# Performance work log

Measured on AMD Instinct MI355X. Metric: run time of the kernel, lower is better.

## Reference

```python
import jax, jax.numpy as jnp
import numpy as np

B, T, C = 2, 2048, 1024
N_HEAD = 16
HEAD_DIM = C // N_HEAD

def setup_inputs() -> dict:
    key = jax.random.key(0)
    k1, k2, k3 = jax.random.split(key, 3)
    x = jax.random.normal(k1, (B, T, C), dtype=jnp.float32)
    # Dense kernel init scale ~ 1/sqrt(fan_in) for stable softmax
    w_attn = jax.random.normal(k2, (C, 3 * C), dtype=jnp.float32) / np.sqrt(C)
    w_proj = jax.random.normal(k3, (C, C), dtype=jnp.float32) / np.sqrt(C)
    return {"x": x, "w_attn": w_attn, "w_proj": w_proj}

def reference(x, w_attn, w_proj):
    Bc, Tc, Cc = x.shape
    # QKV projection (use_bias=False)
    qkv = x @ w_attn  # [B, T, 3C]
    q, k, v = jnp.split(qkv, 3, axis=-1)
    # [B, T, C] -> [B, H, T, D]
    def heads(a):
        return a.reshape(Bc, Tc, N_HEAD, HEAD_DIM).swapaxes(1, 2)
    q, k, v = heads(q), heads(k), heads(v)
    scale = 1.0 / jnp.sqrt(jnp.asarray(HEAD_DIM, dtype=x.dtype))
    attn = jnp.einsum('bhqd,bhkd->bhqk', q, k) * scale  # [B, H, T, T]
    attn = jax.nn.softmax(attn, axis=-1)
    # dropout=0.0 / deterministic -> identity
    y = jnp.einsum('bhqk,bhkd->bhqd', attn, v)  # [B, H, T, D]
    y = y.swapaxes(1, 2).reshape(Bc, Tc, Cc)
    return y @ w_proj  # output projection, no bias, dropout identity
```

## Files before the change

kernel.cpp:

```cpp
#include <hip/hip_runtime.h>
#include <hip/hip_bf16.h>

#define B_   2
#define T_   2048
#define C_   1024
#define NH_  16
#define HD_  64

typedef __attribute__((ext_vector_type(8))) short short8;
typedef __attribute__((ext_vector_type(4))) float float4_;
typedef __attribute__((ext_vector_type(4))) _Float16 half4_;
typedef __attribute__((ext_vector_type(2))) __fp16  fp16x2;

static __device__ __forceinline__ unsigned short f2bf(float f) {
    union { float f; unsigned u; } v; v.f = f;
    unsigned r = v.u + 0x7fffu + ((v.u >> 16) & 1u);
    return (unsigned short)(r >> 16);
}
static __device__ __forceinline__ float bf2f(unsigned short b) {
    union { unsigned u; float f; } v; v.u = (unsigned)b << 16;
    return v.f;
}

static __device__ __forceinline__ void g2l16(const void* g, void* l) {
    __builtin_amdgcn_global_load_lds(
        (const __attribute__((address_space(1))) void*)g,
        (__attribute__((address_space(3))) void*)l, 16, 0, 0);
}

__global__ __launch_bounds__(256) void conv_bf16(
    const float* __restrict__ in, unsigned short* __restrict__ out, int n8)
{
    int i = blockIdx.x * 256 + threadIdx.x;
    if (i >= n8) return;
    const float4* p = (const float4*)in + (size_t)i * 2;
    float4 a = p[0], b = p[1];
    short8 o;
    o[0]=f2bf(a.x); o[1]=f2bf(a.y); o[2]=f2bf(a.z); o[3]=f2bf(a.w);
    o[4]=f2bf(b.x); o[5]=f2bf(b.y); o[6]=f2bf(b.z); o[7]=f2bf(b.w);
    *((short8*)out + i) = o;
}

__global__ __launch_bounds__(256) void tconv2(
    const float* __restrict__ inA, unsigned short* __restrict__ outA, int CcA, int ys,
    const float* __restrict__ inB, unsigned short* __restrict__ outB, int CcB)
{
    __shared__ __align__(16) unsigned short Ts[64][72];
    const int t = threadIdx.x;
    const int R = 1024;
    const float* in; unsigned short* out; int Cc, c0;
    if ((int)blockIdx.y < ys) { in = inA; out = outA; Cc = CcA; c0 = blockIdx.y * 64; }
    else                      { in = inB; out = outB; Cc = CcB; c0 = (blockIdx.y - ys) * 64; }
    const int r0 = blockIdx.x * 64;
    #pragma unroll
    for (int cc = 0; cc < 2; ++cc) {
        int c = cc * 256 + t;
        int r = c >> 3, col = (c & 7) * 8;
        const float* p = in + (size_t)(r0 + r) * Cc + c0 + col;
        #pragma unroll
        for (int i = 0; i < 8; ++i) Ts[col + i][r] = f2bf(p[i]);
    }
    __syncthreads();
    #pragma unroll
    for (int cc = 0; cc < 2; ++cc) {
        int c = cc * 256 + t;
        int cr = c >> 3, oc = (c & 7) * 8;
        uint4 v = *(const uint4*)(&Ts[cr][oc]);
        *(uint4*)(out + (size_t)(c0 + cr) * R + r0 + oc) = v;
    }
}

__global__ __launch_bounds__(256) void vtrans(
    const unsigned short* __restrict__ qkv, unsigned short* __restrict__ vt)
{
    __shared__ __align__(16) unsigned short Ts[64][72];
    const int t = threadIdx.x;
    const int t0 = blockIdx.x * 64, bh = blockIdx.y;
    const int b = bh >> 4, h = bh & 15;
    const unsigned short* Vg = qkv + (size_t)b * T_ * (3 * C_) + 2 * C_ + h * HD_;
    #pragma unroll
    for (int cc = 0; cc < 2; ++cc) {
        int c = cc * 256 + t;
        int r = c >> 3, col = (c & 7) * 8;
        uint4 v = *(const uint4*)(Vg + (size_t)(t0 + r) * (3 * C_) + col);
        const unsigned short* vs = (const unsigned short*)&v;
        #pragma unroll
        for (int i = 0; i < 8; ++i) {
            union { __fp16 h; unsigned short u; } cv;
            cv.h = (__fp16)bf2f(vs[i]);
            Ts[col + i][r] = cv.u;
        }
    }
    __syncthreads();
    #pragma unroll
    for (int cc = 0; cc < 2; ++cc) {
        int c = cc * 256 + t;
        int dr = c >> 3, tc = (c & 7) * 8;
        uint4 v = *(const uint4*)(&Ts[dr][tc]);
        *(uint4*)(vt + ((size_t)bh * HD_ + dr) * T_ + t0 + tc) = v;
    }
}

template <bool C_F32, int BM>
__global__ __launch_bounds__(256) void gemm_bt(
    const unsigned short* __restrict__ A,
    const unsigned short* __restrict__ Bt,
    void* __restrict__ Cv, int M, int N, int K)
{
    __shared__ __align__(16) unsigned short As[BM * 32];
    __shared__ __align__(16) unsigned short Bs[128 * 32];
    const int t = threadIdx.x, lane = t & 63, w = t >> 6;
    const int quad = lane >> 4, ln = lane & 15;
    const int bm = blockIdx.x, bn = blockIdx.y;
    constexpr int NI = (BM == 128) ? 4 : 2;
    const int mw = (BM == 128) ? (w & 1) * 64 : 0;
    const int nw = (BM == 128) ? (w >> 1) * 64 : w * 32;
    float4_ acc[4][NI] = {};

    constexpr int AROWS = BM / 4;
    const unsigned short* Ag = A  + (size_t)(bm * BM + w * AROWS + (lane >> 2)) * K + (lane & 3) * 8;
    const unsigned short* Bg = Bt + (size_t)(bn * 128 + w * 32 + (lane >> 2)) * K + (lane & 3) * 8;
    unsigned short* lA = &As[(w * AROWS) * 32 + lane * 8];
    unsigned short* lB = &Bs[(w * 32) * 32 + lane * 8];

    for (int k0 = 0; k0 < K; k0 += 32) {
        g2l16(Ag + k0, lA);
        if (BM == 128) g2l16(Ag + (size_t)16 * K + k0, lA + 16 * 32);
        g2l16(Bg + k0,                  lB);
        g2l16(Bg + (size_t)16 * K + k0, lB + 16 * 32);
        __syncthreads();
        short8 a[4], b[NI];
        #pragma unroll
        for (int i = 0; i < 4; ++i)
            a[i] = *(const short8*)(&As[(mw + i * 16 + ln) * 32 + quad * 8]);
        #pragma unroll
        for (int i = 0; i < NI; ++i)
            b[i] = *(const short8*)(&Bs[(nw + i * 16 + ln) * 32 + quad * 8]);
        #pragma unroll
        for (int mi = 0; mi < 4; ++mi)
            #pragma unroll
            for (int ni = 0; ni < NI; ++ni)
                acc[mi][ni] = __builtin_amdgcn_mfma_f32_16x16x32_bf16(
                    a[mi], b[ni], acc[mi][ni], 0, 0, 0);
        __syncthreads();
    }

    const int row0 = bm * BM + mw + quad * 4;
    const int col0 = bn * 128 + nw + ln;
    #pragma unroll
    for (int mi = 0; mi < 4; ++mi)
        #pragma unroll
        for (int ni = 0; ni < NI; ++ni)
            #pragma unroll
            for (int i = 0; i < 4; ++i) {
                size_t idx = (size_t)(row0 + mi * 16 + i) * N + col0 + ni * 16;
                if (C_F32) ((float*)Cv)[idx] = acc[mi][ni][i];
                else       ((unsigned short*)Cv)[idx] = f2bf(acc[mi][ni][i]);
            }
}

__global__ __launch_bounds__(256) void attn(
    const unsigned short* __restrict__ qkv,
    const unsigned short* __restrict__ vt,
    unsigned short* __restrict__ Y)
{
    __shared__ __align__(16) unsigned short Qs[64][72];
    __shared__ __align__(16) unsigned short Ks[64][72];
    __shared__ __align__(16) unsigned short Vs[64][72];

    const int t = threadIdx.x;
    const int qt = blockIdx.x, bh = blockIdx.y;
    const int b = bh >> 4, h = bh & 15;
    const int lane = t & 63, w = t >> 6;
    const int quad = lane >> 4, ln = lane & 15;

    const unsigned short* Qg  = qkv + (size_t)b * T_ * (3 * C_) + (size_t)h * HD_;
    const unsigned short* Kg  = Qg + C_;
    const unsigned short* Vtg = vt + (size_t)bh * HD_ * T_;

    const int r0 = t >> 3, c0v = (t & 7) * 8;
    const int r1 = (256 + t) >> 3, c1v = c0v;

    *(uint4*)(&Qs[r0][c0v]) = *(const uint4*)(Qg + (size_t)(qt * 64 + r0) * (3 * C_) + c0v);
    *(uint4*)(&Qs[r1][c1v]) = *(const uint4*)(Qg + (size_t)(qt * 64 + r1) * (3 * C_) + c1v);

    uint4 kr0 = *(const uint4*)(Kg + (size_t)r0 * (3 * C_) + c0v);
    uint4 kr1 = *(const uint4*)(Kg + (size_t)r1 * (3 * C_) + c1v);
    uint4 vr0 = *(const uint4*)(Vtg + (size_t)r0 * T_ + c0v);
    uint4 vr1 = *(const uint4*)(Vtg + (size_t)r1 * T_ + c1v);

    __syncthreads();

    short8 qf[2];
    #pragma unroll
    for (int dh = 0; dh < 2; ++dh)
        qf[dh] = *(const short8*)(&Qs[w * 16 + ln][dh * 32 + quad * 8]);

    float4_ ot[4] = {};
    float ls = 0.f;
    const float scale = 0.125f;
    const float M0 = 8.0f;

    for (int kt = 0; kt < T_ / 64; ++kt) {
        if (kt) __syncthreads();
        *(uint4*)(&Ks[r0][c0v]) = kr0;
        *(uint4*)(&Ks[r1][c1v]) = kr1;
        *(uint4*)(&Vs[r0][c0v]) = vr0;
        *(uint4*)(&Vs[r1][c1v]) = vr1;
        __syncthreads();

        if (kt + 1 < T_ / 64) {
            int kb = (kt + 1) * 64;
            kr0 = *(const uint4*)(Kg + (size_t)(kb + r0) * (3 * C_) + c0v);
            kr1 = *(const uint4*)(Kg + (size_t)(kb + r1) * (3 * C_) + c1v);
            vr0 = *(const uint4*)(Vtg + (size_t)r0 * T_ + kb + c0v);
            vr1 = *(const uint4*)(Vtg + (size_t)r1 * T_ + kb + c1v);
        }

        float4_ st[4] = {};
        #pragma unroll
        for (int ct = 0; ct < 4; ++ct)
            #pragma unroll
            for (int dh = 0; dh < 2; ++dh) {
                short8 kb2 = *(const short8*)(&Ks[ct * 16 + ln][dh * 32 + quad * 8]);
                st[ct] = __builtin_amdgcn_mfma_f32_16x16x32_bf16(kb2, qf[dh], st[ct], 0, 0, 0);
            }

        half4_ pf[4];
        #pragma unroll
        for (int ct = 0; ct < 4; ++ct) {
            float p0 = __expf(st[ct][0] * scale - M0);
            float p1 = __expf(st[ct][1] * scale - M0);
            float p2 = __expf(st[ct][2] * scale - M0);
            float p3 = __expf(st[ct][3] * scale - M0);
            ls += (p0 + p1) + (p2 + p3);
            union { fp16x2 h2[2]; half4_ h4; } u;
            u.h2[0] = __builtin_amdgcn_cvt_pkrtz(p0, p1);
            u.h2[1] = __builtin_amdgcn_cvt_pkrtz(p2, p3);
            pf[ct] = u.h4;
        }

        #pragma unroll
        for (int dt = 0; dt < 4; ++dt)
            #pragma unroll
            for (int ct = 0; ct < 4; ++ct) {
                half4_ va = *(const half4_*)(&Vs[dt * 16 + ln][ct * 16 + quad * 4]);
                ot[dt] = __builtin_amdgcn_mfma_f32_16x16x16f16(va, pf[ct], ot[dt], 0, 0, 0);
            }
    }

    ls += __shfl_xor(ls, 16, 64);
    ls += __shfl_xor(ls, 32, 64);

    unsigned short* Yr = Y + ((size_t)b * T_ + qt * 64 + w * 16 + ln) * C_ + h * HD_;
    float inv = 1.0f / ls;
    #pragma unroll
    for (int dt = 0; dt < 4; ++dt)
        #pragma unroll
        for (int i = 0; i < 4; ++i)
            Yr[dt * 16 + quad * 4 + i] = f2bf(ot[dt][i] * inv);
}

extern "C" void kernel_launch(void* const* d_in, const int* in_sizes, int n_in,
                              void* d_out, int out_size, void* d_ws, size_t ws_size,
                              hipStream_t stream)
{
    const float* x      = (const float*)d_in[0];
    const float* w_attn = (const float*)d_in[1];
    const float* w_proj = (const float*)d_in[2];
    float* out = (float*)d_out;

    unsigned short* qkv = (unsigned short*)d_ws;
    unsigned short* y   = qkv + (size_t)4096 * 3072;
    unsigned short* wTa = y   + (size_t)4096 * 1024;
    unsigned short* wTp = wTa + (size_t)3072 * 1024;
    unsigned short* vt  = wTp + (size_t)1024 * 1024;
    unsigned short* xb  = y;

    conv_bf16<<<2048, 256, 0, stream>>>(x, xb, 4096 * 1024 / 8);
    tconv2<<<dim3(16, 64), 256, 0, stream>>>(w_attn, wTa, 3072, 48, w_proj, wTp, 1024);

    gemm_bt<false, 128><<<dim3(32, 24), 256, 0, stream>>>(xb, wTa, qkv, 4096, 3072, 1024);
    vtrans<<<dim3(32, 32), 256, 0, stream>>>(qkv, vt);
    attn<<<dim3(32, 32), 256, 0, stream>>>(qkv, vt, y);
    gemm_bt<true, 64><<<dim3(64, 8), 256, 0, stream>>>(y, wTp, out, 4096, 1024, 1024);
}
```

Measured before the change: 213.9 us.

## Merge prep conversions into one launch and fuse V transpose into QKV GEMM epilogue

```diff
diff --git a/kernel.cpp b/kernel.cpp
--- a/kernel.cpp
+++ b/kernel.cpp
@@ -11,6 +11,7 @@
 typedef __attribute__((ext_vector_type(4))) float float4_;
 typedef __attribute__((ext_vector_type(4))) _Float16 half4_;
 typedef __attribute__((ext_vector_type(2))) __fp16  fp16x2;
+typedef __attribute__((ext_vector_type(4))) unsigned short ushort4_;
 
 static __device__ __forceinline__ unsigned short f2bf(float f) {
     union { float f; unsigned u; } v; v.f = f;
@@ -28,30 +29,30 @@
         (__attribute__((address_space(3))) void*)l, 16, 0, 0);
 }
 
-__global__ __launch_bounds__(256) void conv_bf16(
-    const float* __restrict__ in, unsigned short* __restrict__ out, int n8)
-{
-    int i = blockIdx.x * 256 + threadIdx.x;
-    if (i >= n8) return;
-    const float4* p = (const float4*)in + (size_t)i * 2;
-    float4 a = p[0], b = p[1];
-    short8 o;
-    o[0]=f2bf(a.x); o[1]=f2bf(a.y); o[2]=f2bf(a.z); o[3]=f2bf(a.w);
-    o[4]=f2bf(b.x); o[5]=f2bf(b.y); o[6]=f2bf(b.z); o[7]=f2bf(b.w);
-    *((short8*)out + i) = o;
-}
-
-__global__ __launch_bounds__(256) void tconv2(
-    const float* __restrict__ inA, unsigned short* __restrict__ outA, int CcA, int ys,
-    const float* __restrict__ inB, unsigned short* __restrict__ outB, int CcB)
-{
+__global__ __launch_bounds__(256) void prep(
+    const float* __restrict__ x,      unsigned short* __restrict__ xb,
+    const float* __restrict__ wA,     unsigned short* __restrict__ wTa,
+    const float* __restrict__ wP,     unsigned short* __restrict__ wTp)
+{
+    const int t = threadIdx.x;
+    int blk = blockIdx.x;
+    if (blk < 2048) {
+        int i = blk * 256 + t;
+        const float4* p = (const float4*)x + (size_t)i * 2;
+        float4 a = p[0], b = p[1];
+        short8 o;
+        o[0]=f2bf(a.x); o[1]=f2bf(a.y); o[2]=f2bf(a.z); o[3]=f2bf(a.w);
+        o[4]=f2bf(b.x); o[5]=f2bf(b.y); o[6]=f2bf(b.z); o[7]=f2bf(b.w);
+        *((short8*)xb + i) = o;
+        return;
+    }
+    blk -= 2048;
+    const float* in; unsigned short* out; int Cc;
+    if (blk < 16 * 48) { in = wA; out = wTa; Cc = 3072; }
+    else               { blk -= 16 * 48; in = wP; out = wTp; Cc = 1024; }
+    const int r0 = (blk % 16) * 64, c0 = (blk / 16) * 64;
+    const int R = 1024;
     __shared__ __align__(16) unsigned short Ts[64][72];
-    const int t = threadIdx.x;
-    const int R = 1024;
-    const float* in; unsigned short* out; int Cc, c0;
-    if ((int)blockIdx.y < ys) { in = inA; out = outA; Cc = CcA; c0 = blockIdx.y * 64; }
-    else                      { in = inB; out = outB; Cc = CcB; c0 = (blockIdx.y - ys) * 64; }
-    const int r0 = blockIdx.x * 64;
     #pragma unroll
     for (int cc = 0; cc < 2; ++cc) {
         int c = cc * 256 + t;
@@ -70,42 +71,12 @@
     }
 }
 
-__global__ __launch_bounds__(256) void vtrans(
-    const unsigned short* __restrict__ qkv, unsigned short* __restrict__ vt)
-{
-    __shared__ __align__(16) unsigned short Ts[64][72];
-    const int t = threadIdx.x;
-    const int t0 = blockIdx.x * 64, bh = blockIdx.y;
-    const int b = bh >> 4, h = bh & 15;
-    const unsigned short* Vg = qkv + (size_t)b * T_ * (3 * C_) + 2 * C_ + h * HD_;
-    #pragma unroll
-    for (int cc = 0; cc < 2; ++cc) {
-        int c = cc * 256 + t;
-        int r = c >> 3, col = (c & 7) * 8;
-        uint4 v = *(const uint4*)(Vg + (size_t)(t0 + r) * (3 * C_) + col);
-        const unsigned short* vs = (const unsigned short*)&v;
-        #pragma unroll
-        for (int i = 0; i < 8; ++i) {
-            union { __fp16 h; unsigned short u; } cv;
-            cv.h = (__fp16)bf2f(vs[i]);
-            Ts[col + i][r] = cv.u;
-        }
-    }
-    __syncthreads();
-    #pragma unroll
-    for (int cc = 0; cc < 2; ++cc) {
-        int c = cc * 256 + t;
-        int dr = c >> 3, tc = (c & 7) * 8;
-        uint4 v = *(const uint4*)(&Ts[dr][tc]);
-        *(uint4*)(vt + ((size_t)bh * HD_ + dr) * T_ + t0 + tc) = v;
-    }
-}
-
-template <bool C_F32, int BM>
+template <bool C_F32, int BM, bool WRITE_VT>
 __global__ __launch_bounds__(256) void gemm_bt(
     const unsigned short* __restrict__ A,
     const unsigned short* __restrict__ Bt,
-    void* __restrict__ Cv, int M, int N, int K)
+    void* __restrict__ Cv, unsigned short* __restrict__ vt,
+    int M, int N, int K)
 {
     __shared__ __align__(16) unsigned short As[BM * 32];
     __shared__ __align__(16) unsigned short Bs[128 * 32];
@@ -150,13 +121,23 @@
     #pragma unroll
     for (int mi = 0; mi < 4; ++mi)
         #pragma unroll
-        for (int ni = 0; ni < NI; ++ni)
+        for (int ni = 0; ni < NI; ++ni) {
             #pragma unroll
             for (int i = 0; i < 4; ++i) {
                 size_t idx = (size_t)(row0 + mi * 16 + i) * N + col0 + ni * 16;
                 if (C_F32) ((float*)Cv)[idx] = acc[mi][ni][i];
                 else       ((unsigned short*)Cv)[idx] = f2bf(acc[mi][ni][i]);
             }
+            if (WRITE_VT && col0 + ni * 16 >= 2 * C_) {
+                int d     = col0 + ni * 16 - 2 * C_;
+                int token = row0 + mi * 16;
+                int b     = token >> 11, tloc = token & 2047;
+                union { fp16x2 h2[2]; ushort4_ u4; } pk;
+                pk.h2[0] = __builtin_amdgcn_cvt_pkrtz(acc[mi][ni][0], acc[mi][ni][1]);
+                pk.h2[1] = __builtin_amdgcn_cvt_pkrtz(acc[mi][ni][2], acc[mi][ni][3]);
+                *(ushort4_*)(vt + ((size_t)b * 1024 + d) * T_ + tloc) = pk.u4;
+            }
+        }
 }
 
 __global__ __launch_bounds__(256) void attn(
@@ -277,11 +258,11 @@
     unsigned short* vt  = wTp + (size_t)1024 * 1024;
     unsigned short* xb  = y;
 
-    conv_bf16<<<2048, 256, 0, stream>>>(x, xb, 4096 * 1024 / 8);
-    tconv2<<<dim3(16, 64), 256, 0, stream>>>(w_attn, wTa, 3072, 48, w_proj, wTp, 1024);
-
-    gemm_bt<false, 128><<<dim3(32, 24), 256, 0, stream>>>(xb, wTa, qkv, 4096, 3072, 1024);
-    vtrans<<<dim3(32, 32), 256, 0, stream>>>(qkv, vt);
+    prep<<<2048 + 16 * 48 + 16 * 16, 256, 0, stream>>>(x, xb, w_attn, wTa, w_proj, wTp);
+
+    gemm_bt<false, 128, true><<<dim3(32, 24), 256, 0, stream>>>(
+        xb, wTa, qkv, vt, 4096, 3072, 1024);
     attn<<<dim3(32, 32), 256, 0, stream>>>(qkv, vt, y);
-    gemm_bt<true, 64><<<dim3(64, 8), 256, 0, stream>>>(y, wTp, out, 4096, 1024, 1024);
-}
+    gemm_bt<true, 64, false><<<dim3(64, 8), 256, 0, stream>>>(
+        y, wTp, out, nullptr, 4096, 1024, 1024);
+}
```

After: 204.6 us. 4.4% less time.
